# Performance work log

Measured on AMD Instinct MI355X. Metric: run time of the kernel, lower is better.

Reference implementation:

```python
import jax, jax.numpy as jnp
import numpy as np
import math

D_MODEL = 1024
N_HEADS = 16
D_K = D_MODEL // N_HEADS
HIDDEN = 4096
R_SOFTPLUS_0 = 1.442695041
EPS = 1e-6


def setup_inputs() -> dict:
    key = jax.random.key(0)
    ks = jax.random.split(key, 16)
    B, S = 4, 2048
    s = 0.02
    inp = {
        "inputs": jax.random.normal(ks[0], (B, S, D_MODEL), jnp.float32),
        "mask": jnp.zeros((1, 1, S, S), jnp.float32),
        # RmsNorm (direct_scale=True -> init 1.0)
        "rms_scale": jnp.ones((D_MODEL,), jnp.float32),
        # attention projections (torch Linear: y = x @ W.T + b)
        "Wq": jax.random.normal(ks[1], (D_MODEL, D_MODEL), jnp.float32) * s,
        "bq": jnp.zeros((D_MODEL,), jnp.float32),
        "Wk": jax.random.normal(ks[2], (D_MODEL, D_MODEL), jnp.float32) * s,
        "bk": jnp.zeros((D_MODEL,), jnp.float32),
        "Wv": jax.random.normal(ks[3], (D_MODEL, D_MODEL), jnp.float32) * s,
        "bv": jnp.zeros((D_MODEL,), jnp.float32),
        "per_dim_scale": jnp.zeros((D_K,), jnp.float32),
        "Wpost": jax.random.normal(ks[4], (D_MODEL, D_MODEL), jnp.float32) * s,
        "bpost": jnp.zeros((D_MODEL,), jnp.float32),
        # FFN LayerNorm (direct_scale=False -> scale param init 0, effective 1+scale)
        "ln_scale": jnp.zeros((D_MODEL,), jnp.float32),
        "ln_bias": jnp.zeros((D_MODEL,), jnp.float32),
        "W1": jax.random.normal(ks[5], (HIDDEN, D_MODEL), jnp.float32) * s,
        "b1": jnp.zeros((HIDDEN,), jnp.float32),
        "W2": jax.random.normal(ks[6], (D_MODEL, HIDDEN), jnp.float32) * s,
        "b2": jnp.zeros((D_MODEL,), jnp.float32),
    }
    return inp


def _rms_norm(x, scale):
    ms = jnp.mean(x * x, axis=-1, keepdims=True)
    return x * jax.lax.rsqrt(ms + EPS) * scale


def _layer_norm(x, scale, bias):
    mean = jnp.mean(x, axis=-1, keepdims=True)
    var = jnp.mean((x - mean) ** 2, axis=-1, keepdims=True)
    return (x - mean) * jax.lax.rsqrt(var + EPS) * (1.0 + scale) + bias


def reference(inputs, mask, rms_scale, Wq, bq, Wk, bk, Wv, bv, per_dim_scale,
              Wpost, bpost, ln_scale, ln_bias, W1, b1, W2, b2):
    B, S, _ = inputs.shape
    x = _rms_norm(inputs, rms_scale)
    # projections -> [B, H, S, Dk]
    def split_heads(t):
        return t.reshape(B, S, N_HEADS, D_K).transpose(0, 2, 1, 3)
    q = split_heads(x @ Wq.T + bq)
    k = split_heads(x @ Wk.T + bk)
    v = split_heads(x @ Wv.T + bv)
    # PerDimScale: (r_softplus_0 / sqrt(d_k)) * softplus(param)
    scale = (R_SOFTPLUS_0 / math.sqrt(D_K)) * jax.nn.softplus(per_dim_scale)
    q = q * scale
    attn = jnp.einsum("bhqd,bhkd->bhqk", q, k) + mask
    attn = jax.nn.softmax(attn, axis=-1)
    out = jnp.einsum("bhqk,bhkd->bhqd", attn, v)
    out = out.transpose(0, 2, 1, 3).reshape(B, S, D_MODEL)
    attn_out = out @ Wpost.T + bpost
    h = attn_out + inputs  # residual (dropout=0)
    # FeedForward with pre-LayerNorm and residual
    y = _layer_norm(h, ln_scale, ln_bias)
    y = jax.nn.relu(y @ W1.T + b1)
    y = y @ W2.T + b2
    return y + h
```

## Files before the change

### kernel.cpp

```cpp
#include <hip/hip_runtime.h>
#include <hip/hip_bf16.h>

typedef unsigned short u16;
typedef __attribute__((ext_vector_type(8))) short short8;
typedef __attribute__((ext_vector_type(4))) float floatx4;

#define R_PDS 0.18033688f

__device__ __forceinline__ float bf2f(u16 u) {
    union { float f; unsigned int i; } c; c.i = ((unsigned int)u) << 16; return c.f;
}
__device__ __forceinline__ u16 f2b(float f) {
    union { float f; unsigned int i; } c; c.f = f;
    unsigned int r = c.i + 0x7fffu + ((c.i >> 16) & 1u);
    return (u16)(r >> 16);
}
__device__ __forceinline__ unsigned int pk2(float a, float b) {
    __hip_bfloat162 h = __float22bfloat162_rn(float2{a, b});
    unsigned int u; __builtin_memcpy(&u, &h, 4); return u;
}

__device__ __forceinline__ void async16(const u16* g, u16* l) {
    __builtin_amdgcn_global_load_lds(
        (const __attribute__((address_space(1))) unsigned int*)g,
        (__attribute__((address_space(3))) unsigned int*)l, 16, 0, 0);
}

__global__ __launch_bounds__(256) void f2b_k(const float* __restrict__ in, u16* __restrict__ out) {
    int i = blockIdx.x * 256 + threadIdx.x;
    float4 v = ((const float4*)in)[i];
    uint2 w;
    w.x = pk2(v.x, v.y);
    w.y = pk2(v.z, v.w);
    ((uint2*)out)[i] = w;
}

__global__ void zero_flag_k(int* f) { *f = 0; }

__global__ __launch_bounds__(256) void mask_any_k(const float* __restrict__ mask, int* flag) {
    int i = blockIdx.x * 256 + threadIdx.x;
    uint4 u = ((const uint4*)mask)[i];
    unsigned int v = (u.x | u.y | u.z | u.w) & 0x7fffffffu;
    if (v) atomicOr(flag, 1);
}

__global__ __launch_bounds__(256) void rmsnorm_k(const float* __restrict__ in,
                                                 const float* __restrict__ gscale,
                                                 u16* __restrict__ out) {
    int row = blockIdx.x;
    int t = threadIdx.x, lane = t & 63, wave = t >> 6;
    const float* x = in + (size_t)row * 1024;
    float4 v = *(const float4*)(x + t * 4);
    float ss = v.x*v.x + v.y*v.y + v.z*v.z + v.w*v.w;
    for (int o = 1; o < 64; o <<= 1) ss += __shfl_xor(ss, o, 64);
    __shared__ float red[4];
    if (lane == 0) red[wave] = ss;
    __syncthreads();
    float tot = red[0] + red[1] + red[2] + red[3];
    float inv = rsqrtf(tot * (1.0f / 1024.0f) + 1e-6f);
    float4 s = *(const float4*)(gscale + t * 4);
    uint2 w;
    w.x = pk2(v.x * inv * s.x, v.y * inv * s.y);
    w.y = pk2(v.z * inv * s.z, v.w * inv * s.w);
    *(uint2*)(out + (size_t)row * 1024 + t * 4) = w;
}

__global__ __launch_bounds__(256) void layernorm_k(const u16* __restrict__ in,
                                                   const float* __restrict__ gs,
                                                   const float* __restrict__ gb,
                                                   u16* __restrict__ out) {
    int row = blockIdx.x;
    int t = threadIdx.x, lane = t & 63, wave = t >> 6;
    const u16* x = in + (size_t)row * 1024;
    uint2 u = *(const uint2*)(x + t * 4);
    float v0 = bf2f((u16)(u.x & 0xffff)), v1 = bf2f((u16)(u.x >> 16));
    float v2 = bf2f((u16)(u.y & 0xffff)), v3 = bf2f((u16)(u.y >> 16));
    float s1 = v0 + v1 + v2 + v3;
    float s2 = v0*v0 + v1*v1 + v2*v2 + v3*v3;
    for (int o = 1; o < 64; o <<= 1) { s1 += __shfl_xor(s1, o, 64); s2 += __shfl_xor(s2, o, 64); }
    __shared__ float r1[4], r2[4];
    if (lane == 0) { r1[wave] = s1; r2[wave] = s2; }
    __syncthreads();
    float mean = (r1[0] + r1[1] + r1[2] + r1[3]) * (1.0f / 1024.0f);
    float var  = (r2[0] + r2[1] + r2[2] + r2[3]) * (1.0f / 1024.0f) - mean * mean;
    var = fmaxf(var, 0.0f);
    float inv = rsqrtf(var + 1e-6f);
    float4 sc = *(const float4*)(gs + t * 4);
    float4 bb = *(const float4*)(gb + t * 4);
    uint2 w;
    w.x = pk2((v0 - mean) * inv * (1.0f + sc.x) + bb.x,
              (v1 - mean) * inv * (1.0f + sc.y) + bb.y);
    w.y = pk2((v2 - mean) * inv * (1.0f + sc.z) + bb.z,
              (v3 - mean) * inv * (1.0f + sc.w) + bb.w);
    *(uint2*)(out + (size_t)row * 1024 + t * 4) = w;
}

template <int EPI, bool OUTF32, bool RESF32>
__global__ __launch_bounds__(256) void gemm_bt_k(const u16* __restrict__ A,
                                                 const u16* __restrict__ B,
                                                 const float* __restrict__ bias,
                                                 const void* __restrict__ res,
                                                 void* __restrict__ Cv,
                                                 int M, int N, int K) {
    __shared__ __align__(16) u16 As[4096];
    __shared__ __align__(16) u16 Bs[4096];
    const int t = threadIdx.x, wave = t >> 6, lane = t & 63;
    const int quad = lane >> 4, ln = lane & 15;
    const int m0 = blockIdx.y * 128, n0 = blockIdx.x * 128;
    const int wm = (wave >> 1) * 64, wn = (wave & 1) * 64;

    floatx4 acc[4][4];
    for (int mt = 0; mt < 4; mt++) for (int nt = 0; nt < 4; nt++) acc[mt][nt] = (floatx4)0.0f;

    const int c0 = t, c1 = t + 256;
    const u16* Ap0 = A + (size_t)(m0 + (c0 >> 2)) * K + (c0 & 3) * 8;
    const u16* Ap1 = A + (size_t)(m0 + (c1 >> 2)) * K + (c1 & 3) * 8;
    const u16* Bp0 = B + (size_t)(n0 + (c0 >> 2)) * K + (c0 & 3) * 8;
    const u16* Bp1 = B + (size_t)(n0 + (c1 >> 2)) * K + (c1 & 3) * 8;
    u16* AsW0 = As + wave * 512;
    u16* AsW1 = As + 2048 + wave * 512;
    u16* BsW0 = Bs + wave * 512;
    u16* BsW1 = Bs + 2048 + wave * 512;

    for (int kt = 0; kt < K; kt += 32) {
        __syncthreads();
        async16(Ap0 + kt, AsW0);
        async16(Ap1 + kt, AsW1);
        async16(Bp0 + kt, BsW0);
        async16(Bp1 + kt, BsW1);
        __syncthreads();
        short8 af[4], bfr[4];
        for (int mt = 0; mt < 4; mt++)
            af[mt] = *(const short8*)&As[(wm + mt * 16 + ln) * 32 + quad * 8];
        for (int nt = 0; nt < 4; nt++)
            bfr[nt] = *(const short8*)&Bs[(wn + nt * 16 + ln) * 32 + quad * 8];
        for (int mt = 0; mt < 4; mt++)
            for (int nt = 0; nt < 4; nt++)
                acc[mt][nt] = __builtin_amdgcn_mfma_f32_16x16x32_bf16(af[mt], bfr[nt], acc[mt][nt], 0, 0, 0);
    }

    for (int nt = 0; nt < 4; nt++) {
        int col = n0 + wn + nt * 16 + ln;
        float bv = bias[col];
        for (int mt = 0; mt < 4; mt++) {
            for (int r = 0; r < 4; r++) {
                int row = m0 + wm + mt * 16 + quad * 4 + r;
                float v = acc[mt][nt][r] + bv;
                if (EPI == 1) v = fmaxf(v, 0.0f);
                if (EPI == 2) {
                    if (RESF32) v += ((const float*)res)[(size_t)row * N + col];
                    else        v += bf2f(((const u16*)res)[(size_t)row * N + col]);
                }
                if (OUTF32) ((float*)Cv)[(size_t)row * N + col] = v;
                else        ((u16*)Cv)[(size_t)row * N + col] = f2b(v);
            }
        }
    }
}

__global__ __launch_bounds__(256) void gemm_qkv_k(const u16* __restrict__ A,
                                                  const u16* __restrict__ B,
                                                  const float* __restrict__ bq,
                                                  const float* __restrict__ bk,
                                                  const float* __restrict__ bv,
                                                  const float* __restrict__ pds,
                                                  u16* __restrict__ C) {
    const int K = 1024, N = 3072;
    __shared__ __align__(16) u16 As[4096];
    __shared__ __align__(16) u16 Bs[4096];
    const int t = threadIdx.x, wave = t >> 6, lane = t & 63;
    const int quad = lane >> 4, ln = lane & 15;
    const int m0 = blockIdx.y * 128, n0 = blockIdx.x * 128;
    const int wm = (wave >> 1) * 64, wn = (wave & 1) * 64;

    floatx4 acc[4][4];
    for (int mt = 0; mt < 4; mt++) for (int nt = 0; nt < 4; nt++) acc[mt][nt] = (floatx4)0.0f;

    const int c0 = t, c1 = t + 256;
    const u16* Ap0 = A + (size_t)(m0 + (c0 >> 2)) * K + (c0 & 3) * 8;
    const u16* Ap1 = A + (size_t)(m0 + (c1 >> 2)) * K + (c1 & 3) * 8;
    const u16* Bp0 = B + (size_t)(n0 + (c0 >> 2)) * K + (c0 & 3) * 8;
    const u16* Bp1 = B + (size_t)(n0 + (c1 >> 2)) * K + (c1 & 3) * 8;
    u16* AsW0 = As + wave * 512;
    u16* AsW1 = As + 2048 + wave * 512;
    u16* BsW0 = Bs + wave * 512;
    u16* BsW1 = Bs + 2048 + wave * 512;

    for (int kt = 0; kt < K; kt += 32) {
        __syncthreads();
        async16(Ap0 + kt, AsW0);
        async16(Ap1 + kt, AsW1);
        async16(Bp0 + kt, BsW0);
        async16(Bp1 + kt, BsW1);
        __syncthreads();
        short8 af[4], bfr[4];
        for (int mt = 0; mt < 4; mt++)
            af[mt] = *(const short8*)&As[(wm + mt * 16 + ln) * 32 + quad * 8];
        for (int nt = 0; nt < 4; nt++)
            bfr[nt] = *(const short8*)&Bs[(wn + nt * 16 + ln) * 32 + quad * 8];
        for (int mt = 0; mt < 4; mt++)
            for (int nt = 0; nt < 4; nt++)
                acc[mt][nt] = __builtin_amdgcn_mfma_f32_16x16x32_bf16(af[mt], bfr[nt], acc[mt][nt], 0, 0, 0);
    }

    for (int nt = 0; nt < 4; nt++) {
        int col = n0 + wn + nt * 16 + ln;
        float bv_, sc = 1.0f;
        if (col < 1024) {
            bv_ = bq[col];
            float xp = pds[col & 63];
            float sp = (xp > 20.0f) ? xp : log1pf(__expf(xp));
            sc = R_PDS * sp;
        } else if (col < 2048) bv_ = bk[col - 1024];
        else                   bv_ = bv[col - 2048];
        for (int mt = 0; mt < 4; mt++)
            for (int r = 0; r < 4; r++) {
                int row = m0 + wm + mt * 16 + quad * 4 + r;
                C[(size_t)row * N + col] = f2b((acc[mt][nt][r] + bv_) * sc);
            }
    }
}

__global__ __launch_bounds__(256) void transpose_v_k(const u16* __restrict__ qkv, u16* __restrict__ vT) {
    __shared__ u16 tile[64][65];
    int st = blockIdx.x, bh = blockIdx.y;
    int b = bh >> 4, h = bh & 15;
    const u16* vb = qkv + (size_t)(b * 2048 + st * 64) * 3072 + 2048 + h * 64;
    int t = threadIdx.x;
    for (int i = t; i < 4096; i += 256) {
        int s = i >> 6, d = i & 63;
        tile[s][d] = vb[(size_t)s * 3072 + d];
    }
    __syncthreads();
    u16* ob = vT + (size_t)bh * 131072 + st * 64;
    for (int i = t; i < 4096; i += 256) {
        int d = i >> 6, s = i & 63;
        ob[(size_t)d * 2048 + s] = tile[s][d];
    }
}

__global__ __launch_bounds__(256) void attn_k(const u16* __restrict__ qkv,
                                              const u16* __restrict__ vT,
                                              const float* __restrict__ mask,
                                              const int* __restrict__ flag,
                                              u16* __restrict__ o) {
    __shared__ __align__(16) u16 Qs[64][72];
    __shared__ __align__(16) u16 Ks[64][72];
    __shared__ __align__(16) u16 Vs[64][72];
    __shared__ __align__(16) u16 Ps[64][72];

    const int t = threadIdx.x, wave = t >> 6, lane = t & 63;
    const int quad = lane >> 4, ln = lane & 15;
    const int qt = blockIdx.x, bh = blockIdx.y;
    const int b = bh >> 4, h = bh & 15;
    const int q0 = qt * 64;

    const u16* qb = qkv + (size_t)(b * 2048 + q0) * 3072 + h * 64;
    for (int c = t; c < 512; c += 256) {
        int row = c >> 3, seg = c & 7;
        *(uint4*)&Qs[row][seg * 8] = *(const uint4*)(qb + (size_t)row * 3072 + seg * 8);
    }
    __syncthreads();

    short8 qf[2];
    for (int ks = 0; ks < 2; ks++)
        qf[ks] = *(const short8*)&Qs[wave * 16 + ln][ks * 32 + quad * 8];

    short8 ones_f;
    for (int i = 0; i < 8; i++) ones_f[i] = (short)0x3F80;

    floatx4 acc_o[4], acc_l = (floatx4)0.0f;
    for (int dt = 0; dt < 4; dt++) acc_o[dt] = (floatx4)0.0f;

    const int mflag = *flag;
    const u16* kb = qkv + (size_t)(b * 2048) * 3072 + 1024 + h * 64;
    const u16* vg = vT + (size_t)bh * 131072;

    for (int kv0 = 0; kv0 < 2048; kv0 += 64) {
        __syncthreads();
        for (int c = t; c < 512; c += 256) {
            int row = c >> 3, seg = c & 7;
            *(uint4*)&Ks[row][seg * 8] = *(const uint4*)(kb + (size_t)(kv0 + row) * 3072 + seg * 8);
            *(uint4*)&Vs[row][seg * 8] = *(const uint4*)(vg + (size_t)row * 2048 + kv0 + seg * 8);
        }
        __syncthreads();

        floatx4 acc_s[4];
        for (int nt = 0; nt < 4; nt++) acc_s[nt] = (floatx4)0.0f;
        for (int ks = 0; ks < 2; ks++)
            for (int nt = 0; nt < 4; nt++) {
                short8 bfr = *(const short8*)&Ks[nt * 16 + ln][ks * 32 + quad * 8];
                acc_s[nt] = __builtin_amdgcn_mfma_f32_16x16x32_bf16(qf[ks], bfr, acc_s[nt], 0, 0, 0);
            }
        if (mflag) {
            for (int nt = 0; nt < 4; nt++)
                for (int r = 0; r < 4; r++) {
                    int qr = q0 + wave * 16 + quad * 4 + r;
                    int kc = kv0 + nt * 16 + ln;
                    acc_s[nt][r] += mask[(size_t)qr * 2048 + kc];
                }
        }

        int prow = wave * 16 + quad * 4;
        for (int nt = 0; nt < 4; nt++) {
            unsigned int u01 = pk2(__expf(fminf(acc_s[nt][0], 60.0f)),
                                   __expf(fminf(acc_s[nt][1], 60.0f)));
            unsigned int u23 = pk2(__expf(fminf(acc_s[nt][2], 60.0f)),
                                   __expf(fminf(acc_s[nt][3], 60.0f)));
            Ps[prow + 0][nt * 16 + ln] = (u16)(u01 & 0xffff);
            Ps[prow + 1][nt * 16 + ln] = (u16)(u01 >> 16);
            Ps[prow + 2][nt * 16 + ln] = (u16)(u23 & 0xffff);
            Ps[prow + 3][nt * 16 + ln] = (u16)(u23 >> 16);
        }

        for (int ks = 0; ks < 2; ks++) {
            short8 a = *(const short8*)&Ps[wave * 16 + ln][ks * 32 + quad * 8];
            acc_l = __builtin_amdgcn_mfma_f32_16x16x32_bf16(a, ones_f, acc_l, 0, 0, 0);
            for (int dt = 0; dt < 4; dt++) {
                short8 bfr = *(const short8*)&Vs[dt * 16 + ln][ks * 32 + quad * 8];
                acc_o[dt] = __builtin_amdgcn_mfma_f32_16x16x32_bf16(a, bfr, acc_o[dt], 0, 0, 0);
            }
        }
    }

    u16* ob = o + (size_t)(b * 2048 + q0) * 1024 + h * 64;
    for (int r = 0; r < 4; r++) {
        float inv = 1.0f / acc_l[r];
        int row = wave * 16 + quad * 4 + r;
        for (int dt = 0; dt < 4; dt++)
            ob[(size_t)row * 1024 + dt * 16 + ln] = f2b(acc_o[dt][r] * inv);
    }
}

extern "C" void kernel_launch(void* const* d_in, const int* in_sizes, int n_in,
                              void* d_out, int out_size, void* d_ws, size_t ws_size,
                              hipStream_t stream) {
    const float* inp    = (const float*)d_in[0];
    const float* mask   = (const float*)d_in[1];
    const float* rms_s  = (const float*)d_in[2];
    const float* Wq     = (const float*)d_in[3];
    const float* bq     = (const float*)d_in[4];
    const float* Wk     = (const float*)d_in[5];
    const float* bk     = (const float*)d_in[6];
    const float* Wv     = (const float*)d_in[7];
    const float* bv     = (const float*)d_in[8];
    const float* pds    = (const float*)d_in[9];
    const float* Wpost  = (const float*)d_in[10];
    const float* bpost  = (const float*)d_in[11];
    const float* ln_s   = (const float*)d_in[12];
    const float* ln_b   = (const float*)d_in[13];
    const float* W1     = (const float*)d_in[14];
    const float* b1     = (const float*)d_in[15];
    const float* W2     = (const float*)d_in[16];
    const float* b2     = (const float*)d_in[17];
    float* out = (float*)d_out;

    char* w = (char*)d_ws;
    const size_t MB = 1u << 20;
    u16* W1b   = (u16*)(w + 0 * MB);
    u16* W2b   = (u16*)(w + 8 * MB);
    u16* qkv   = (u16*)(w + 16 * MB);
    u16* x     = (u16*)(w + 64 * MB);
    u16* o     = (u16*)(w + 64 * MB);
    u16* Wqkvb = (u16*)(w + 80 * MB);
    u16* Wpb   = (u16*)(w + 86 * MB);
    u16* yln   = (u16*)(w + 80 * MB);
    u16* vT    = (u16*)(w + 96 * MB);
    u16* hb    = (u16*)(w + 96 * MB);
    u16* f1    = (u16*)(w + 16 * MB);
    int* flag  = (int*)(w + 112 * MB);

    f2b_k<<<1024, 256, 0, stream>>>(Wq, Wqkvb);
    f2b_k<<<1024, 256, 0, stream>>>(Wk, Wqkvb + 1024 * 1024);
    f2b_k<<<1024, 256, 0, stream>>>(Wv, Wqkvb + 2 * 1024 * 1024);
    f2b_k<<<1024, 256, 0, stream>>>(Wpost, Wpb);
    f2b_k<<<4096, 256, 0, stream>>>(W1, W1b);
    f2b_k<<<4096, 256, 0, stream>>>(W2, W2b);

    zero_flag_k<<<1, 1, 0, stream>>>(flag);
    mask_any_k<<<4096, 256, 0, stream>>>(mask, flag);

    rmsnorm_k<<<8192, 256, 0, stream>>>(inp, rms_s, x);

    gemm_qkv_k<<<dim3(24, 64), 256, 0, stream>>>(x, Wqkvb, bq, bk, bv, pds, qkv);

    transpose_v_k<<<dim3(32, 64), 256, 0, stream>>>(qkv, vT);

    attn_k<<<dim3(32, 64), 256, 0, stream>>>(qkv, vT, mask, flag, o);

    gemm_bt_k<2, false, true><<<dim3(8, 64), 256, 0, stream>>>(o, Wpb, bpost, inp, hb, 8192, 1024, 1024);

    layernorm_k<<<8192, 256, 0, stream>>>(hb, ln_s, ln_b, yln);

    gemm_bt_k<1, false, true><<<dim3(32, 64), 256, 0, stream>>>(yln, W1b, b1, nullptr, f1, 8192, 4096, 1024);
    gemm_bt_k<2, true, false><<<dim3(8, 64), 256, 0, stream>>>(f1, W2b, b2, hb, out, 8192, 1024, 4096);
}
```

Measured before the change: 632.2 us.

## Fuse weight conversion launches, prefetch K/V into registers, use exp2 softmax

Merges the six weight-conversion kernels and the flag reset into one launch, which cuts launch overhead. In the attention kernel, the next K/V tile is loaded into registers while the current tile is computed, so global-load latency overlaps with MFMA work. The separate P buffer now reuses the Q shared buffer to lower LDS use. The log2e factor is folded into the query scale and the mask so that exp2 can replace exp. The exp clamp changes to 80 in the log2 domain, which shifts the overflow threshold slightly.

```diff
diff --git a/kernel.cpp b/kernel.cpp
--- a/kernel.cpp
+++ b/kernel.cpp
@@ -6,6 +6,7 @@
 typedef __attribute__((ext_vector_type(4))) float floatx4;
 
 #define R_PDS 0.18033688f
+#define LOG2E 1.4426950408889634f
 
 __device__ __forceinline__ float bf2f(u16 u) {
     union { float f; unsigned int i; } c; c.i = ((unsigned int)u) << 16; return c.f;
@@ -26,16 +27,26 @@
         (__attribute__((address_space(3))) unsigned int*)l, 16, 0, 0);
 }
 
-__global__ __launch_bounds__(256) void f2b_k(const float* __restrict__ in, u16* __restrict__ out) {
-    int i = blockIdx.x * 256 + threadIdx.x;
-    float4 v = ((const float4*)in)[i];
-    uint2 w;
-    w.x = pk2(v.x, v.y);
-    w.y = pk2(v.z, v.w);
-    ((uint2*)out)[i] = w;
-}
-
-__global__ void zero_flag_k(int* f) { *f = 0; }
+__global__ __launch_bounds__(256) void f2b_all_k(const float* __restrict__ Wq, const float* __restrict__ Wk,
+                                                 const float* __restrict__ Wv, const float* __restrict__ Wp,
+                                                 const float* __restrict__ W1, const float* __restrict__ W2,
+                                                 u16* __restrict__ Wqkvb, u16* __restrict__ Wpb,
+                                                 u16* __restrict__ W1b,  u16* __restrict__ W2b,
+                                                 int* flag) {
+    int bid = blockIdx.x;
+    if (bid == 0 && threadIdx.x == 0) *flag = 0;
+    const float* src; u16* dst; int off;
+    if      (bid < 1024) { src = Wq; dst = Wqkvb;                off = bid; }
+    else if (bid < 2048) { src = Wk; dst = Wqkvb + 1024 * 1024;  off = bid - 1024; }
+    else if (bid < 3072) { src = Wv; dst = Wqkvb + 2048 * 1024;  off = bid - 2048; }
+    else if (bid < 4096) { src = Wp; dst = Wpb;                  off = bid - 3072; }
+    else if (bid < 8192) { src = W1; dst = W1b;                  off = bid - 4096; }
+    else                 { src = W2; dst = W2b;                  off = bid - 8192; }
+    int i = off * 256 + threadIdx.x;
+    float4 v = ((const float4*)src)[i];
+    uint2 w; w.x = pk2(v.x, v.y); w.y = pk2(v.z, v.w);
+    ((uint2*)dst)[i] = w;
+}
 
 __global__ __launch_bounds__(256) void mask_any_k(const float* __restrict__ mask, int* flag) {
     int i = blockIdx.x * 256 + threadIdx.x;
@@ -210,7 +221,7 @@
             bv_ = bq[col];
             float xp = pds[col & 63];
             float sp = (xp > 20.0f) ? xp : log1pf(__expf(xp));
-            sc = R_PDS * sp;
+            sc = R_PDS * sp * LOG2E;
         } else if (col < 2048) bv_ = bk[col - 1024];
         else                   bv_ = bv[col - 2048];
         for (int mt = 0; mt < 4; mt++)
@@ -244,10 +255,9 @@
                                               const float* __restrict__ mask,
                                               const int* __restrict__ flag,
                                               u16* __restrict__ o) {
-    __shared__ __align__(16) u16 Qs[64][72];
+    __shared__ __align__(16) u16 QPs[64][72];
     __shared__ __align__(16) u16 Ks[64][72];
     __shared__ __align__(16) u16 Vs[64][72];
-    __shared__ __align__(16) u16 Ps[64][72];
 
     const int t = threadIdx.x, wave = t >> 6, lane = t & 63;
     const int quad = lane >> 4, ln = lane & 15;
@@ -258,13 +268,13 @@
     const u16* qb = qkv + (size_t)(b * 2048 + q0) * 3072 + h * 64;
     for (int c = t; c < 512; c += 256) {
         int row = c >> 3, seg = c & 7;
-        *(uint4*)&Qs[row][seg * 8] = *(const uint4*)(qb + (size_t)row * 3072 + seg * 8);
+        *(uint4*)&QPs[row][seg * 8] = *(const uint4*)(qb + (size_t)row * 3072 + seg * 8);
     }
     __syncthreads();
 
     short8 qf[2];
     for (int ks = 0; ks < 2; ks++)
-        qf[ks] = *(const short8*)&Qs[wave * 16 + ln][ks * 32 + quad * 8];
+        qf[ks] = *(const short8*)&QPs[wave * 16 + ln][ks * 32 + quad * 8];
 
     short8 ones_f;
     for (int i = 0; i < 8; i++) ones_f[i] = (short)0x3F80;
@@ -276,14 +286,32 @@
     const u16* kb = qkv + (size_t)(b * 2048) * 3072 + 1024 + h * 64;
     const u16* vg = vT + (size_t)bh * 131072;
 
+    const int r0 = t >> 3, s0 = (t & 7) * 8;
+    const u16* kp0 = kb + (size_t)r0 * 3072 + s0;
+    const u16* kp1 = kb + (size_t)(r0 + 32) * 3072 + s0;
+    const u16* vp0 = vg + (size_t)r0 * 2048 + s0;
+    const u16* vp1 = vg + (size_t)(r0 + 32) * 2048 + s0;
+
+    uint4 kr0 = *(const uint4*)(kp0);
+    uint4 kr1 = *(const uint4*)(kp1);
+    uint4 vr0 = *(const uint4*)(vp0);
+    uint4 vr1 = *(const uint4*)(vp1);
+
     for (int kv0 = 0; kv0 < 2048; kv0 += 64) {
         __syncthreads();
-        for (int c = t; c < 512; c += 256) {
-            int row = c >> 3, seg = c & 7;
-            *(uint4*)&Ks[row][seg * 8] = *(const uint4*)(kb + (size_t)(kv0 + row) * 3072 + seg * 8);
-            *(uint4*)&Vs[row][seg * 8] = *(const uint4*)(vg + (size_t)row * 2048 + kv0 + seg * 8);
+        *(uint4*)&Ks[r0][s0]      = kr0;
+        *(uint4*)&Ks[r0 + 32][s0] = kr1;
+        *(uint4*)&Vs[r0][s0]      = vr0;
+        *(uint4*)&Vs[r0 + 32][s0] = vr1;
+        __syncthreads();
+        if (kv0 + 64 < 2048) {
+            size_t ko = (size_t)(kv0 + 64) * 3072;
+            int    vo = kv0 + 64;
+            kr0 = *(const uint4*)(kp0 + ko);
+            kr1 = *(const uint4*)(kp1 + ko);
+            vr0 = *(const uint4*)(vp0 + vo);
+            vr1 = *(const uint4*)(vp1 + vo);
         }
-        __syncthreads();
 
         floatx4 acc_s[4];
         for (int nt = 0; nt < 4; nt++) acc_s[nt] = (floatx4)0.0f;
@@ -297,24 +325,24 @@
                 for (int r = 0; r < 4; r++) {
                     int qr = q0 + wave * 16 + quad * 4 + r;
                     int kc = kv0 + nt * 16 + ln;
-                    acc_s[nt][r] += mask[(size_t)qr * 2048 + kc];
+                    acc_s[nt][r] += mask[(size_t)qr * 2048 + kc] * LOG2E;
                 }
         }
 
         int prow = wave * 16 + quad * 4;
         for (int nt = 0; nt < 4; nt++) {
-            unsigned int u01 = pk2(__expf(fminf(acc_s[nt][0], 60.0f)),
-                                   __expf(fminf(acc_s[nt][1], 60.0f)));
-            unsigned int u23 = pk2(__expf(fminf(acc_s[nt][2], 60.0f)),
-                                   __expf(fminf(acc_s[nt][3], 60.0f)));
-            Ps[prow + 0][nt * 16 + ln] = (u16)(u01 & 0xffff);
-            Ps[prow + 1][nt * 16 + ln] = (u16)(u01 >> 16);
-            Ps[prow + 2][nt * 16 + ln] = (u16)(u23 & 0xffff);
-            Ps[prow + 3][nt * 16 + ln] = (u16)(u23 >> 16);
+            unsigned int u01 = pk2(__builtin_amdgcn_exp2f(fminf(acc_s[nt][0], 80.0f)),
+                                   __builtin_amdgcn_exp2f(fminf(acc_s[nt][1], 80.0f)));
+            unsigned int u23 = pk2(__builtin_amdgcn_exp2f(fminf(acc_s[nt][2], 80.0f)),
+                                   __builtin_amdgcn_exp2f(fminf(acc_s[nt][3], 80.0f)));
+            QPs[prow + 0][nt * 16 + ln] = (u16)(u01 & 0xffff);
+            QPs[prow + 1][nt * 16 + ln] = (u16)(u01 >> 16);
+            QPs[prow + 2][nt * 16 + ln] = (u16)(u23 & 0xffff);
+            QPs[prow + 3][nt * 16 + ln] = (u16)(u23 >> 16);
         }
 
         for (int ks = 0; ks < 2; ks++) {
-            short8 a = *(const short8*)&Ps[wave * 16 + ln][ks * 32 + quad * 8];
+            short8 a = *(const short8*)&QPs[wave * 16 + ln][ks * 32 + quad * 8];
             acc_l = __builtin_amdgcn_mfma_f32_16x16x32_bf16(a, ones_f, acc_l, 0, 0, 0);
             for (int dt = 0; dt < 4; dt++) {
                 short8 bfr = *(const short8*)&Vs[dt * 16 + ln][ks * 32 + quad * 8];
@@ -370,14 +398,7 @@
     u16* f1    = (u16*)(w + 16 * MB);
     int* flag  = (int*)(w + 112 * MB);
 
-    f2b_k<<<1024, 256, 0, stream>>>(Wq, Wqkvb);
-    f2b_k<<<1024, 256, 0, stream>>>(Wk, Wqkvb + 1024 * 1024);
-    f2b_k<<<1024, 256, 0, stream>>>(Wv, Wqkvb + 2 * 1024 * 1024);
-    f2b_k<<<1024, 256, 0, stream>>>(Wpost, Wpb);
-    f2b_k<<<4096, 256, 0, stream>>>(W1, W1b);
-    f2b_k<<<4096, 256, 0, stream>>>(W2, W2b);
-
-    zero_flag_k<<<1, 1, 0, stream>>>(flag);
+    f2b_all_k<<<12288, 256, 0, stream>>>(Wq, Wk, Wv, Wpost, W1, W2, Wqkvb, Wpb, W1b, W2b, flag);
     mask_any_k<<<4096, 256, 0, stream>>>(mask, flag);
 
     rmsnorm_k<<<8192, 256, 0, stream>>>(inp, rms_s, x);
```

Result: faster. 614.6 us (-2.8%).
